# Kernel optimization log

Measured on AMD Instinct MI355X. Metric: run time of the kernel, lower is better.

Reference implementation:

```python
import jax, jax.numpy as jnp
import numpy as np

HIDDEN = 256        # hidden width of the dynamics MLP
N_ODE_STEPS = 2     # fixed-step RK4 steps over t_sim = [0, 1] per block


def setup_inputs() -> dict:
    key = jax.random.key(0)
    ks = jax.random.split(key, 8)
    S, B, N, d, p, block = 2, 8, 2048, 64, 32, 8
    s = jax.random.normal(ks[0], (S, B, N, d), jnp.float32)
    # strictly increasing time grid so delta = diff(t) > 0
    dt_raw = jax.random.uniform(ks[1], (S, B, block + 1), jnp.float32)
    t = jnp.cumsum(0.05 + 0.1 * dt_raw, axis=2)
    Phi = jax.random.normal(ks[2], (S, B, N, p), jnp.float32)
    b = 0.1 * jax.random.normal(ks[3], (S, B, N, d), jnp.float32)
    W1 = jax.random.normal(ks[4], (d + p, HIDDEN), jnp.float32) / np.sqrt(d + p).astype(np.float32)
    b1 = jnp.zeros((HIDDEN,), jnp.float32)
    W2 = jax.random.normal(ks[5], (HIDDEN, d), jnp.float32) / np.sqrt(HIDDEN).astype(np.float32)
    b2 = jnp.zeros((d,), jnp.float32)
    return dict(s=s, t=t, Phi=Phi, b=b, W1=W1, b1=b1, W2=W2, b2=b2)


def _dyn(x, Phi, b, W1, b1, W2, b2):
    # f(t, x, Phi, b): MLP over per-node latent + spatial features, plus forcing b.
    h = jnp.tanh(jnp.einsum('sbnf,fh->sbnh', jnp.concatenate([x, Phi], axis=-1), W1) + b1)
    return jnp.einsum('sbnh,hd->sbnd', h, W2) + b2 + b


def reference(s, t, Phi, b, W1, b1, W2, b2):
    S, B, N, d = s.shape
    block = t.shape[2] - 1
    delta = jnp.diff(t, axis=2)                      # (S, B, block)
    deltas = jnp.moveaxis(delta, 2, 0)[..., None, None]  # (block, S, B, 1, 1)
    dt = 1.0 / N_ODE_STEPS

    def g(x, dlt):
        # scaled dynamics: f(t, x, Phi, b) * delta  (time-rescaled to [0, 1])
        return _dyn(x, Phi, b, W1, b1, W2, b2) * dlt

    def block_step(x, dlt):
        def rk4(x, _):
            k1 = g(x, dlt)
            k2 = g(x + 0.5 * dt * k1, dlt)
            k3 = g(x + 0.5 * dt * k2, dlt)
            k4 = g(x + dt * k3, dlt)
            return x + (dt / 6.0) * (k1 + 2.0 * k2 + 2.0 * k3 + k4), None
        x, _ = jax.lax.scan(rk4, x, None, length=N_ODE_STEPS)
        return x, x

    _, s_stack = jax.lax.scan(block_step, s, deltas)  # (block, S, B, N, d)
    # 'S B block N d -> S (B block) N d'
    return jnp.moveaxis(s_stack, 0, 2).reshape(S, B * block, N, d)
```

## Files before the change

kernel.cpp:

```cpp
#include <hip/hip_runtime.h>

typedef short  short8   __attribute__((ext_vector_type(8)));
typedef float  floatx4  __attribute__((ext_vector_type(4)));
typedef unsigned int uintx2 __attribute__((ext_vector_type(2)));

#define LOG2E_X2 2.8853900817779268f

__device__ __forceinline__ float tanh_fast(float a) {
    float e = __builtin_amdgcn_exp2f(a * LOG2E_X2);
    return 1.0f - 2.0f * __builtin_amdgcn_rcpf(1.0f + e);
}

__device__ __forceinline__ unsigned short bf16rne(float f) {
    unsigned u = __float_as_uint(f);
    u += 0x7FFFu + ((u >> 16) & 1u);
    return (unsigned short)(u >> 16);
}

#if __has_builtin(__builtin_amdgcn_cvt_pk_bf16_f32)
__device__ __forceinline__ unsigned pk2(float a, float b) {
    auto r = __builtin_amdgcn_cvt_pk_bf16_f32(a, b);
    unsigned u; __builtin_memcpy(&u, &r, 4);
    return u;
}
#else
__device__ __forceinline__ unsigned pk2(float a, float b) {
    unsigned r;
    asm("v_cvt_pk_bf16_f32 %0, %1, %2" : "=v"(r) : "v"(a), "v"(b));
    return r;
}
#endif

__global__ __launch_bounds__(256, 2) void ode_mfma(
    const float* __restrict__ s_in,  const float* __restrict__ t_in,
    const float* __restrict__ phi_in,const float* __restrict__ bfr_in,
    const float* __restrict__ w1_in, const float* __restrict__ b1_in,
    const float* __restrict__ w2_in, const float* __restrict__ b2_in,
    float* __restrict__ out)
{
    const int tid  = threadIdx.x;
    const int wv   = tid >> 6;
    const int lane = tid & 63;
    const int l15  = lane & 15;
    const int q    = lane >> 4;
    const int wg   = blockIdx.x;
    const int sb   = wg >> 5;
    const int n0   = (wg & 31) << 6;
    const int rowg0 = sb * 2048 + n0;

    __shared__ __align__(16) unsigned short Atile[64][104];
    __shared__ __align__(16) unsigned short Hs[64][264];
    __shared__ __align__(16) float b1s[256];
    __shared__ float dls[8];

    const int d0 = wv * 16 + q * 4;

    short8 w1f[4][3];
#pragma unroll
    for (int ht = 0; ht < 4; ++ht)
#pragma unroll
        for (int kk = 0; kk < 3; ++kk) {
            short8 f;
#pragma unroll
            for (int j = 0; j < 8; ++j) {
                int k = kk * 32 + q * 8 + j;
                int hc = (wv * 4 + ht) * 16 + l15;
                f[j] = (short)bf16rne(w1_in[k * 256 + hc]);
            }
            w1f[ht][kk] = f;
        }
    short8 w2f[8];
#pragma unroll
    for (int kk = 0; kk < 8; ++kk) {
        short8 f;
#pragma unroll
        for (int j = 0; j < 8; ++j) {
            int k = kk * 32 + q * 8 + j;
            f[j] = (short)bf16rne(w2_in[k * 64 + wv * 16 + l15]);
        }
        w2f[kk] = f;
    }

    floatx4 xv[4], kacc[4], fbv[4];
    {
        const floatx4 b2v = *(const floatx4*)(b2_in + d0);
#pragma unroll
        for (int rt = 0; rt < 4; ++rt) {
            int rg = rowg0 + rt * 16 + l15;
            xv[rt]  = *(const floatx4*)(s_in   + rg * 64 + d0);
            fbv[rt] = b2v + *(const floatx4*)(bfr_in + rg * 64 + d0);
            uintx2 px = { pk2(xv[rt][0], xv[rt][1]), pk2(xv[rt][2], xv[rt][3]) };
            *(uintx2*)&Atile[rt * 16 + l15][d0] = px;
        }
    }
#pragma unroll
    for (int it = 0; it < 2; ++it) {
        int c2 = tid * 2 + it;
        int row = c2 >> 3, cc = c2 & 7;
        floatx4 p = *(const floatx4*)(phi_in + (rowg0 + row) * 32 + cc * 4);
        uintx2 px = { pk2(p[0], p[1]), pk2(p[2], p[3]) };
        *(uintx2*)&Atile[row][64 + cc * 4] = px;
    }
    if (tid < 64) *(floatx4*)&b1s[tid * 4] = *(const floatx4*)(b1_in + tid * 4);
    if (tid < 8)  dls[tid] = t_in[sb * 9 + tid + 1] - t_in[sb * 9 + tid];

    __syncthreads();

#define DO_G1(RT0)                                                              \
    {                                                                           \
        floatx4 bbf[4];                                                         \
        _Pragma("unroll")                                                       \
        for (int ht = 0; ht < 4; ++ht)                                          \
            bbf[ht] = *(const floatx4*)&b1s[(wv * 4 + ht) * 16 + q * 4];        \
        floatx4 acc1[4][2];                                                     \
        {                                                                       \
            short8 xb[2];                                                       \
            _Pragma("unroll")                                                   \
            for (int r2 = 0; r2 < 2; ++r2)                                      \
                xb[r2] = *(const short8*)&Atile[(RT0 + r2) * 16 + l15][q * 8];  \
            _Pragma("unroll")                                                   \
            for (int ht = 0; ht < 4; ++ht)                                      \
                _Pragma("unroll")                                               \
                for (int r2 = 0; r2 < 2; ++r2)                                  \
                    acc1[ht][r2] = __builtin_amdgcn_mfma_f32_16x16x32_bf16(     \
                        w1f[ht][0], xb[r2], bbf[ht], 0, 0, 0);                  \
        }                                                                       \
        _Pragma("unroll")                                                       \
        for (int kk = 1; kk < 3; ++kk) {                                        \
            short8 xb[2];                                                       \
            _Pragma("unroll")                                                   \
            for (int r2 = 0; r2 < 2; ++r2)                                      \
                xb[r2] = *(const short8*)&Atile[(RT0 + r2) * 16 + l15][kk * 32 + q * 8]; \
            _Pragma("unroll")                                                   \
            for (int ht = 0; ht < 4; ++ht)                                      \
                _Pragma("unroll")                                               \
                for (int r2 = 0; r2 < 2; ++r2)                                  \
                    acc1[ht][r2] = __builtin_amdgcn_mfma_f32_16x16x32_bf16(     \
                        w1f[ht][kk], xb[r2], acc1[ht][r2], 0, 0, 0);            \
        }                                                                       \
        _Pragma("unroll")                                                       \
        for (int ht = 0; ht < 4; ++ht)                                          \
            _Pragma("unroll")                                                   \
            for (int r2 = 0; r2 < 2; ++r2) {                                    \
                uintx2 hp = { pk2(tanh_fast(acc1[ht][r2][0]), tanh_fast(acc1[ht][r2][1])), \
                              pk2(tanh_fast(acc1[ht][r2][2]), tanh_fast(acc1[ht][r2][3])) }; \
                *(uintx2*)&Hs[(RT0 + r2) * 16 + l15][(wv * 4 + ht) * 16 + q * 4] = hp; \
            }                                                                   \
    }

#define DO_G2(RT0)                                                              \
    {                                                                           \
        floatx4 acc2[2];                                                        \
        _Pragma("unroll")                                                       \
        for (int r2 = 0; r2 < 2; ++r2) {                                        \
            short8 hb = *(const short8*)&Hs[(RT0 + r2) * 16 + l15][q * 8];      \
            acc2[r2] = __builtin_amdgcn_mfma_f32_16x16x32_bf16(                 \
                w2f[0], hb, fbv[RT0 + r2], 0, 0, 0);                            \
        }                                                                       \
        _Pragma("unroll")                                                       \
        for (int kk = 1; kk < 8; ++kk)                                          \
            _Pragma("unroll")                                                   \
            for (int r2 = 0; r2 < 2; ++r2) {                                    \
                short8 hb = *(const short8*)&Hs[(RT0 + r2) * 16 + l15][kk * 32 + q * 8]; \
                acc2[r2] = __builtin_amdgcn_mfma_f32_16x16x32_bf16(             \
                    w2f[kk], hb, acc2[r2], 0, 0, 0);                            \
            }                                                                   \
        _Pragma("unroll")                                                       \
        for (int r2 = 0; r2 < 2; ++r2) {                                        \
            const int rt = RT0 + r2;                                            \
            floatx4 kv = acc2[r2] * dlt;                                        \
            floatx4 xe;                                                         \
            if (sub == 0)      { kacc[rt] = kv;            xe = xv[rt] + 0.25f * kv; } \
            else if (sub == 1) { kacc[rt] += 2.0f * kv;    xe = xv[rt] + 0.25f * kv; } \
            else if (sub == 2) { kacc[rt] += 2.0f * kv;    xe = xv[rt] + 0.5f  * kv; } \
            else               { xv[rt] += (kacc[rt] + kv) * (1.0f / 12.0f); xe = xv[rt]; } \
            uintx2 px = { pk2(xe[0], xe[1]), pk2(xe[2], xe[3]) };               \
            *(uintx2*)&Atile[rt * 16 + l15][d0] = px;                           \
        }                                                                       \
        if ((i & 7) == 7) {                                                     \
            const int ob = (sb * 8 + (i >> 3)) * 2048;                          \
            _Pragma("unroll")                                                   \
            for (int r2 = 0; r2 < 2; ++r2) {                                    \
                const int rt = RT0 + r2;                                        \
                *(floatx4*)(out + (size_t)(ob + n0 + rt * 16 + l15) * 64 + d0) = xv[rt]; \
            }                                                                   \
        }                                                                       \
    }

    DO_G1(0)

#pragma unroll 1
    for (int i = 0; i < 64; ++i) {
        const float dlt = dls[i >> 3];
        const int sub = i & 3;
        __syncthreads();
        DO_G2(0)
        DO_G1(2)
        __syncthreads();
        DO_G2(2)
        if (i < 63) { DO_G1(0) }
    }
#undef DO_G1
#undef DO_G2
}

extern "C" void kernel_launch(void* const* d_in, const int* in_sizes, int n_in,
                              void* d_out, int out_size, void* d_ws, size_t ws_size,
                              hipStream_t stream) {
    const float* s_in  = (const float*)d_in[0];
    const float* t_in  = (const float*)d_in[1];
    const float* phi   = (const float*)d_in[2];
    const float* bfr   = (const float*)d_in[3];
    const float* w1    = (const float*)d_in[4];
    const float* b1    = (const float*)d_in[5];
    const float* w2    = (const float*)d_in[6];
    const float* b2    = (const float*)d_in[7];
    ode_mfma<<<512, 256, 0, stream>>>(s_in, t_in, phi, bfr, w1, b1, w2, b2, (float*)d_out);
}
```

Measured before the change: 344.5 us.

## Split hidden dimension across eight waves and fold log2e scaling into W1

Doubles the block to 512 threads (8 waves). Each wave now owns 32 hidden columns in the first layer, and wave halves split the row tiles in the second layer. This halves per-wave register state and MFMA work, to get more waves per CU for latency hiding across the serial RK4 chain. It also pre-multiplies W1 and b1 by 2*log2(e), removing a multiply inside tanh at the cost of slightly different bf16 rounding of W1. The tighter launch bounds (512,4) cap the register budget and may force spills of the resident weight fragments.

```diff
diff --git a/kernel.cpp b/kernel.cpp
--- a/kernel.cpp
+++ b/kernel.cpp
@@ -6,8 +6,8 @@
 
 #define LOG2E_X2 2.8853900817779268f
 
-__device__ __forceinline__ float tanh_fast(float a) {
-    float e = __builtin_amdgcn_exp2f(a * LOG2E_X2);
+__device__ __forceinline__ float tanh_pre(float y) {
+    float e = __builtin_amdgcn_exp2f(y);
     return 1.0f - 2.0f * __builtin_amdgcn_rcpf(1.0f + e);
 }
 
@@ -31,7 +31,7 @@
 }
 #endif
 
-__global__ __launch_bounds__(256, 2) void ode_mfma(
+__global__ __launch_bounds__(512, 4) void ode_mfma(
     const float* __restrict__ s_in,  const float* __restrict__ t_in,
     const float* __restrict__ phi_in,const float* __restrict__ bfr_in,
     const float* __restrict__ w1_in, const float* __restrict__ b1_in,
@@ -39,7 +39,9 @@
     float* __restrict__ out)
 {
     const int tid  = threadIdx.x;
-    const int wv   = tid >> 6;
+    const int w    = tid >> 6;
+    const int wv2  = w & 3;
+    const int rh   = w >> 2;
     const int lane = tid & 63;
     const int l15  = lane & 15;
     const int q    = lane >> 4;
@@ -53,19 +55,19 @@
     __shared__ __align__(16) float b1s[256];
     __shared__ float dls[8];
 
-    const int d0 = wv * 16 + q * 4;
-
-    short8 w1f[4][3];
-#pragma unroll
-    for (int ht = 0; ht < 4; ++ht)
+    const int d0 = wv2 * 16 + q * 4;
+
+    short8 w1f[2][3];
+#pragma unroll
+    for (int ht = 0; ht < 2; ++ht)
 #pragma unroll
         for (int kk = 0; kk < 3; ++kk) {
             short8 f;
 #pragma unroll
             for (int j = 0; j < 8; ++j) {
                 int k = kk * 32 + q * 8 + j;
-                int hc = (wv * 4 + ht) * 16 + l15;
-                f[j] = (short)bf16rne(w1_in[k * 256 + hc]);
+                int hc = w * 32 + ht * 16 + l15;
+                f[j] = (short)bf16rne(w1_in[k * 256 + hc] * LOG2E_X2);
             }
             w1f[ht][kk] = f;
         }
@@ -76,54 +78,55 @@
 #pragma unroll
         for (int j = 0; j < 8; ++j) {
             int k = kk * 32 + q * 8 + j;
-            f[j] = (short)bf16rne(w2_in[k * 64 + wv * 16 + l15]);
+            f[j] = (short)bf16rne(w2_in[k * 64 + wv2 * 16 + l15]);
         }
         w2f[kk] = f;
     }
 
-    floatx4 xv[4], kacc[4], fbv[4];
+    floatx4 xv[2], kacc[2], fbv[2];
     {
         const floatx4 b2v = *(const floatx4*)(b2_in + d0);
 #pragma unroll
-        for (int rt = 0; rt < 4; ++rt) {
+        for (int si = 0; si < 2; ++si) {
+            int rt = si * 2 + rh;
             int rg = rowg0 + rt * 16 + l15;
-            xv[rt]  = *(const floatx4*)(s_in   + rg * 64 + d0);
-            fbv[rt] = b2v + *(const floatx4*)(bfr_in + rg * 64 + d0);
-            uintx2 px = { pk2(xv[rt][0], xv[rt][1]), pk2(xv[rt][2], xv[rt][3]) };
+            xv[si]  = *(const floatx4*)(s_in   + rg * 64 + d0);
+            fbv[si] = b2v + *(const floatx4*)(bfr_in + rg * 64 + d0);
+            uintx2 px = { pk2(xv[si][0], xv[si][1]), pk2(xv[si][2], xv[si][3]) };
             *(uintx2*)&Atile[rt * 16 + l15][d0] = px;
         }
     }
-#pragma unroll
-    for (int it = 0; it < 2; ++it) {
-        int c2 = tid * 2 + it;
-        int row = c2 >> 3, cc = c2 & 7;
+    {
+        int row = tid >> 3, cc = tid & 7;
         floatx4 p = *(const floatx4*)(phi_in + (rowg0 + row) * 32 + cc * 4);
         uintx2 px = { pk2(p[0], p[1]), pk2(p[2], p[3]) };
         *(uintx2*)&Atile[row][64 + cc * 4] = px;
     }
-    if (tid < 64) *(floatx4*)&b1s[tid * 4] = *(const floatx4*)(b1_in + tid * 4);
+    if (tid < 64) {
+        floatx4 v = *(const floatx4*)(b1_in + tid * 4);
+        v *= LOG2E_X2;
+        *(floatx4*)&b1s[tid * 4] = v;
+    }
     if (tid < 8)  dls[tid] = t_in[sb * 9 + tid + 1] - t_in[sb * 9 + tid];
 
     __syncthreads();
 
 #define DO_G1(RT0)                                                              \
     {                                                                           \
-        floatx4 bbf[4];                                                         \
-        _Pragma("unroll")                                                       \
-        for (int ht = 0; ht < 4; ++ht)                                          \
-            bbf[ht] = *(const floatx4*)&b1s[(wv * 4 + ht) * 16 + q * 4];        \
-        floatx4 acc1[4][2];                                                     \
+        floatx4 acc1[2][2];                                                     \
         {                                                                       \
             short8 xb[2];                                                       \
             _Pragma("unroll")                                                   \
             for (int r2 = 0; r2 < 2; ++r2)                                      \
                 xb[r2] = *(const short8*)&Atile[(RT0 + r2) * 16 + l15][q * 8];  \
             _Pragma("unroll")                                                   \
-            for (int ht = 0; ht < 4; ++ht)                                      \
+            for (int ht = 0; ht < 2; ++ht) {                                    \
+                floatx4 bbf = *(const floatx4*)&b1s[w * 32 + ht * 16 + q * 4];  \
                 _Pragma("unroll")                                               \
                 for (int r2 = 0; r2 < 2; ++r2)                                  \
                     acc1[ht][r2] = __builtin_amdgcn_mfma_f32_16x16x32_bf16(     \
-                        w1f[ht][0], xb[r2], bbf[ht], 0, 0, 0);                  \
+                        w1f[ht][0], xb[r2], bbf, 0, 0, 0);                      \
+            }                                                                   \
         }                                                                       \
         _Pragma("unroll")                                                       \
         for (int kk = 1; kk < 3; ++kk) {                                        \
@@ -132,58 +135,50 @@
             for (int r2 = 0; r2 < 2; ++r2)                                      \
                 xb[r2] = *(const short8*)&Atile[(RT0 + r2) * 16 + l15][kk * 32 + q * 8]; \
             _Pragma("unroll")                                                   \
-            for (int ht = 0; ht < 4; ++ht)                                      \
+            for (int ht = 0; ht < 2; ++ht)                                      \
                 _Pragma("unroll")                                               \
                 for (int r2 = 0; r2 < 2; ++r2)                                  \
                     acc1[ht][r2] = __builtin_amdgcn_mfma_f32_16x16x32_bf16(     \
                         w1f[ht][kk], xb[r2], acc1[ht][r2], 0, 0, 0);            \
         }                                                                       \
         _Pragma("unroll")                                                       \
-        for (int ht = 0; ht < 4; ++ht)                                          \
+        for (int ht = 0; ht < 2; ++ht)                                          \
             _Pragma("unroll")                                                   \
             for (int r2 = 0; r2 < 2; ++r2) {                                    \
-                uintx2 hp = { pk2(tanh_fast(acc1[ht][r2][0]), tanh_fast(acc1[ht][r2][1])), \
-                              pk2(tanh_fast(acc1[ht][r2][2]), tanh_fast(acc1[ht][r2][3])) }; \
-                *(uintx2*)&Hs[(RT0 + r2) * 16 + l15][(wv * 4 + ht) * 16 + q * 4] = hp; \
+                uintx2 hp = { pk2(tanh_pre(acc1[ht][r2][0]), tanh_pre(acc1[ht][r2][1])), \
+                              pk2(tanh_pre(acc1[ht][r2][2]), tanh_pre(acc1[ht][r2][3])) }; \
+                *(uintx2*)&Hs[(RT0 + r2) * 16 + l15][w * 32 + ht * 16 + q * 4] = hp; \
             }                                                                   \
     }
 
-#define DO_G2(RT0)                                                              \
+#define DO_G2(SI)                                                               \
     {                                                                           \
-        floatx4 acc2[2];                                                        \
+        const int rt = (SI) * 2 + rh;                                           \
+        floatx4 acc2;                                                           \
+        {                                                                       \
+            short8 hb = *(const short8*)&Hs[rt * 16 + l15][q * 8];              \
+            acc2 = __builtin_amdgcn_mfma_f32_16x16x32_bf16(                     \
+                w2f[0], hb, fbv[SI], 0, 0, 0);                                  \
+        }                                                                       \
         _Pragma("unroll")                                                       \
-        for (int r2 = 0; r2 < 2; ++r2) {                                        \
-            short8 hb = *(const short8*)&Hs[(RT0 + r2) * 16 + l15][q * 8];      \
-            acc2[r2] = __builtin_amdgcn_mfma_f32_16x16x32_bf16(                 \
-                w2f[0], hb, fbv[RT0 + r2], 0, 0, 0);                            \
-        }                                                                       \
-        _Pragma("unroll")                                                       \
-        for (int kk = 1; kk < 8; ++kk)                                          \
-            _Pragma("unroll")                                                   \
-            for (int r2 = 0; r2 < 2; ++r2) {                                    \
-                short8 hb = *(const short8*)&Hs[(RT0 + r2) * 16 + l15][kk * 32 + q * 8]; \
-                acc2[r2] = __builtin_amdgcn_mfma_f32_16x16x32_bf16(             \
-                    w2f[kk], hb, acc2[r2], 0, 0, 0);                            \
-            }                                                                   \
-        _Pragma("unroll")                                                       \
-        for (int r2 = 0; r2 < 2; ++r2) {                                        \
-            const int rt = RT0 + r2;                                            \
-            floatx4 kv = acc2[r2] * dlt;                                        \
+        for (int kk = 1; kk < 8; ++kk) {                                        \
+            short8 hb = *(const short8*)&Hs[rt * 16 + l15][kk * 32 + q * 8];    \
+            acc2 = __builtin_amdgcn_mfma_f32_16x16x32_bf16(                     \
+                w2f[kk], hb, acc2, 0, 0, 0);                                    \
+        }                                                                       \
+        {                                                                       \
+            floatx4 kv = acc2 * dlt;                                            \
             floatx4 xe;                                                         \
-            if (sub == 0)      { kacc[rt] = kv;            xe = xv[rt] + 0.25f * kv; } \
-            else if (sub == 1) { kacc[rt] += 2.0f * kv;    xe = xv[rt] + 0.25f * kv; } \
-            else if (sub == 2) { kacc[rt] += 2.0f * kv;    xe = xv[rt] + 0.5f  * kv; } \
-            else               { xv[rt] += (kacc[rt] + kv) * (1.0f / 12.0f); xe = xv[rt]; } \
+            if (sub == 0)      { kacc[SI] = kv;            xe = xv[SI] + 0.25f * kv; } \
+            else if (sub == 1) { kacc[SI] += 2.0f * kv;    xe = xv[SI] + 0.25f * kv; } \
+            else if (sub == 2) { kacc[SI] += 2.0f * kv;    xe = xv[SI] + 0.5f  * kv; } \
+            else               { xv[SI] += (kacc[SI] + kv) * (1.0f / 12.0f); xe = xv[SI]; } \
             uintx2 px = { pk2(xe[0], xe[1]), pk2(xe[2], xe[3]) };               \
             *(uintx2*)&Atile[rt * 16 + l15][d0] = px;                           \
         }                                                                       \
         if ((i & 7) == 7) {                                                     \
             const int ob = (sb * 8 + (i >> 3)) * 2048;                          \
-            _Pragma("unroll")                                                   \
-            for (int r2 = 0; r2 < 2; ++r2) {                                    \
-                const int rt = RT0 + r2;                                        \
-                *(floatx4*)(out + (size_t)(ob + n0 + rt * 16 + l15) * 64 + d0) = xv[rt]; \
-            }                                                                   \
+            *(floatx4*)(out + (size_t)(ob + n0 + rt * 16 + l15) * 64 + d0) = xv[SI]; \
         }                                                                       \
     }
 
@@ -197,7 +192,7 @@
         DO_G2(0)
         DO_G1(2)
         __syncthreads();
-        DO_G2(2)
+        DO_G2(1)
         if (i < 63) { DO_G1(0) }
     }
 #undef DO_G1
@@ -215,5 +210,5 @@
     const float* b1    = (const float*)d_in[5];
     const float* w2    = (const float*)d_in[6];
     const float* b2    = (const float*)d_in[7];
-    ode_mfma<<<512, 256, 0, stream>>>(s_in, t_in, phi, bfr, w1, b1, w2, b2, (float*)d_out);
-}
+    ode_mfma<<<512, 512, 0, stream>>>(s_in, t_in, phi, bfr, w1, b1, w2, b2, (float*)d_out);
+}
```

Result: faster. 337.8 us (-2.0%).
